# Performance work log

Measured on AMD Instinct MI355X. Metric: run time of the kernel, lower is better.

The kernel has to match this reference:

```python
import jax, jax.numpy as jnp
import numpy as np

NUM_WIRES = 20
BATCH = 32
DIM = 2 ** NUM_WIRES


def setup_inputs() -> dict:
    key = jax.random.key(0)
    k1, k2, k3 = jax.random.split(key, 3)
    state = jax.random.normal(k1, (BATCH, DIM), dtype=jnp.float32)
    state = state / jnp.linalg.norm(state, axis=1, keepdims=True)  # valid quantum states
    params = jax.random.normal(k2, (2 * NUM_WIRES,), dtype=jnp.float32)
    W = jax.random.normal(k3, (1, NUM_WIRES), dtype=jnp.float32) * 0.1
    b = jnp.zeros((1,), dtype=jnp.float32)
    return {"state": state, "params": params, "W": W, "b": b}


def _apply_1q(psi, U, wire):
    # psi: [B, 2^n] complex; apply 2x2 unitary U on `wire` (wire 0 = most significant axis,
    # matching PennyLane's big-endian wire ordering).
    B = psi.shape[0]
    left = 2 ** wire
    psi4 = psi.reshape(B, left, 2, -1)
    psi4 = jnp.einsum('ts,bisj->bitj', U, psi4)
    return psi4.reshape(B, DIM)


def _apply_cnot(psi, ctrl):
    # CNOT on adjacent wires (ctrl, ctrl+1): swap target amplitudes where control=1.
    B = psi.shape[0]
    left = 2 ** ctrl
    psi5 = psi.reshape(B, left, 2, 2, -1)
    top = psi5[:, :, 0]
    bot = psi5[:, :, 1, ::-1]
    return jnp.stack([top, bot], axis=2).reshape(B, DIM)


def _circuit(state, params):
    psi = state.astype(jnp.complex64)
    for i in range(NUM_WIRES):
        # RX(theta_i)
        c = jnp.cos(params[i] / 2).astype(jnp.complex64)
        s = jnp.sin(params[i] / 2)
        RX = jnp.stack([jnp.stack([c, -1j * s]), jnp.stack([-1j * s, c])])
        psi = _apply_1q(psi, RX, i)
        # RY(theta_{i+n})
        c2 = jnp.cos(params[i + NUM_WIRES] / 2).astype(jnp.complex64)
        s2 = jnp.sin(params[i + NUM_WIRES] / 2).astype(jnp.complex64)
        RY = jnp.stack([jnp.stack([c2, -s2]), jnp.stack([s2, c2])])
        psi = _apply_1q(psi, RY, i)
    for i in range(NUM_WIRES - 1):
        psi = _apply_cnot(psi, i)
    # <Z_i> = sum over basis states of |amp|^2 * (+1 if bit_i==0 else -1)
    probs = psi.real ** 2 + psi.imag ** 2  # [B, 2^n] float32
    B = probs.shape[0]
    feats = []
    for i in range(NUM_WIRES):
        p = probs.reshape(B, 2 ** i, 2, -1)
        feats.append(p[:, :, 0].sum(axis=(1, 2)) - p[:, :, 1].sum(axis=(1, 2)))
    return jnp.stack(feats, axis=1)  # [B, n]


def reference(state, params, W, b):
    feats = _circuit(state, params)          # [B, num_wires]
    out = feats @ W.T + b                    # Linear head
    return out.squeeze(-1)                   # [B]
```

## Files before the change

kernel.cpp:

```cpp
#include <hip/hip_runtime.h>
#include <hip/hip_fp16.h>

#define NW    20
#define BATCH 32

struct PkW7 { __half2 a, d, dn, e, en, f, fn, pad; };

__device__ __forceinline__ __half2 pkrtz(float lo, float hi) {
    typedef __fp16 f16x2 __attribute__((ext_vector_type(2)));
    f16x2 v = __builtin_amdgcn_cvt_pkrtz(lo, hi);
    return *reinterpret_cast<__half2*>(&v);
}
__device__ __forceinline__ unsigned h2u(__half2 v) { return *reinterpret_cast<unsigned*>(&v); }
__device__ __forceinline__ __half2 u2h(unsigned v) { return *reinterpret_cast<__half2*>(&v); }

template<int JB>
__device__ __forceinline__ void stage16s(__half2 (&xr)[16], __half2 (&xi)[16], const PkW7 u) {
    #pragma unroll
    for (int base = 0; base < 16; ++base)
        if (!(base & (1 << JB))) {
            const int p = base | (1 << JB);
            __half2 x0r = xr[base], x0i = xi[base], x1r = xr[p], x1i = xi[p];
            xr[base] = __hfma2(u.a, x0r, __hfma2(u.dn, x0i, __hfma2(u.en, x1r, __hmul2(u.f , x1i))));
            xi[base] = __hfma2(u.a, x0i, __hfma2(u.d , x0r, __hfma2(u.en, x1i, __hmul2(u.fn, x1r))));
            xr[p]    = __hfma2(u.e, x0r, __hfma2(u.f , x0i, __hfma2(u.a , x1r, __hmul2(u.d , x1i))));
            xi[p]    = __hfma2(u.e, x0i, __hfma2(u.fn, x0r, __hfma2(u.a , x1i, __hmul2(u.dn, x1r))));
        }
}

__global__ void setupk(const float* __restrict__ params, float* __restrict__ cbuf) {
    int w = threadIdx.x;
    if (w < NW) {
        double s1, c1, s2, c2;
        sincos(0.5 * (double)params[w],      &s1, &c1);
        sincos(0.5 * (double)params[w + NW], &s2, &c2);
        float a = (float)(c1 * c2), d = (float)(s1 * s2);
        float e = (float)(s2 * c1), f = (float)(c2 * s1);
        if (w == 19) {
            cbuf[0] = a * 1024.f; cbuf[1] = d * 1024.f;
            cbuf[2] = e * 1024.f; cbuf[3] = f * 1024.f;
        }
        PkW7 pw;
        pw.a  = __floats2half2_rn( a,  a);
        pw.d  = __floats2half2_rn( d,  d);
        pw.dn = __floats2half2_rn(-d, -d);
        pw.e  = __floats2half2_rn( e,  e);
        pw.en = __floats2half2_rn(-e, -e);
        pw.f  = __floats2half2_rn( f,  f);
        pw.fn = __floats2half2_rn(-f, -f);
        pw.pad = __floats2half2_rn(0.f, 0.f);
        ((PkW7*)(cbuf + 4))[w] = pw;
    }
}

__global__ __launch_bounds__(256, 4) void pass1(const float* __restrict__ state,
                                                const float* __restrict__ cbuf,
                                                uint2* __restrict__ amp) {
    __shared__ __half2 Lr[4224];
    __shared__ __half2 Li[4224];
    const int t     = threadIdx.x;
    const int pr    = blockIdx.x >> 8;
    const int chunk = blockIdx.x & 255;
    const PkW7* PW = (const PkW7*)(cbuf + 4);
    const float a19 = cbuf[0], d19 = cbuf[1], e19 = cbuf[2], f19 = cbuf[3];

    const float4* s0 = (const float4*)(state + ((size_t)pr << 20) + ((size_t)chunk << 12));
    const float4* s1 = (const float4*)((const float*)s0 + ((size_t)16 << 20));

    __half2 xr[16], xi[16];
    #pragma unroll
    for (int k = 0; k < 4; ++k) {
        float4 v0 = s0[k * 256 + t];
        float4 v1 = s1[k * 256 + t];
        float r0a = fmaf(a19, v0.x, -e19 * v0.y), i0a = fmaf( d19, v0.x, -f19 * v0.y);
        float r1a = fmaf(e19, v0.x,  a19 * v0.y), i1a = fmaf(-f19, v0.x, -d19 * v0.y);
        float r0b = fmaf(a19, v1.x, -e19 * v1.y), i0b = fmaf( d19, v1.x, -f19 * v1.y);
        float r1b = fmaf(e19, v1.x,  a19 * v1.y), i1b = fmaf(-f19, v1.x, -d19 * v1.y);
        xr[4*k+0] = pkrtz(r0a, r0b); xi[4*k+0] = pkrtz(i0a, i0b);
        xr[4*k+1] = pkrtz(r1a, r1b); xi[4*k+1] = pkrtz(i1a, i1b);
        r0a = fmaf(a19, v0.z, -e19 * v0.w); i0a = fmaf( d19, v0.z, -f19 * v0.w);
        r1a = fmaf(e19, v0.z,  a19 * v0.w); i1a = fmaf(-f19, v0.z, -d19 * v0.w);
        r0b = fmaf(a19, v1.z, -e19 * v1.w); i0b = fmaf( d19, v1.z, -f19 * v1.w);
        r1b = fmaf(e19, v1.z,  a19 * v1.w); i1b = fmaf(-f19, v1.z, -d19 * v1.w);
        xr[4*k+2] = pkrtz(r0a, r0b); xi[4*k+2] = pkrtz(i0a, i0b);
        xr[4*k+3] = pkrtz(r1a, r1b); xi[4*k+3] = pkrtz(i1a, i1b);
    }
    stage16s<1>(xr, xi, PW[18]);
    stage16s<2>(xr, xi, PW[9]);
    stage16s<3>(xr, xi, PW[8]);
    {
        const int p1 = 4 * t + (t >> 3);
        #pragma unroll
        for (int r = 0; r < 16; ++r) {
            const int a = p1 + (r & 3) + 1056 * (r >> 2);
            Lr[a] = xr[r]; Li[a] = xi[r];
        }
    }
    __syncthreads();

    const int p2 = (t & 3) + 66 * (t >> 2);
    #pragma unroll
    for (int r = 0; r < 16; ++r) {
        const int c = 4 * (r & 3) + 16 * (r >> 2);
        const int a = p2 + c + (c >> 5);
        xr[r] = Lr[a]; xi[r] = Li[a];
    }
    stage16s<0>(xr, xi, PW[17]);
    stage16s<1>(xr, xi, PW[16]);
    stage16s<2>(xr, xi, PW[15]);
    stage16s<3>(xr, xi, PW[14]);
    #pragma unroll
    for (int r = 0; r < 16; ++r) {
        const int c = 4 * (r & 3) + 16 * (r >> 2);
        const int a = p2 + c + (c >> 5);
        Lr[a] = xr[r]; Li[a] = xi[r];
    }
    __syncthreads();

    const int p3 = (t & 63) + ((t & 63) >> 5) + 1056 * (t >> 6);
    #pragma unroll
    for (int r = 0; r < 16; ++r) {
        const int a = p3 + 66 * (r & 3) + 264 * (r >> 2);
        xr[r] = Lr[a]; xi[r] = Li[a];
    }
    stage16s<0>(xr, xi, PW[13]);
    stage16s<1>(xr, xi, PW[12]);
    stage16s<2>(xr, xi, PW[11]);
    stage16s<3>(xr, xi, PW[10]);

    uint2* dst = amp + ((size_t)pr << 20) + ((size_t)chunk << 12);
    const int sbase = (t & 63) + 1024 * (t >> 6);
    #pragma unroll
    for (int r = 0; r < 16; ++r) {
        uint2 w; w.x = h2u(xr[r]); w.y = h2u(xi[r]);
        dst[sbase + 64 * (r & 3) + 256 * (r >> 2)] = w;
    }
}

__global__ __launch_bounds__(256, 4) void pass2(const uint2* __restrict__ amp,
                                                const float* __restrict__ cbuf,
                                                const float* __restrict__ Wv,
                                                float* __restrict__ pws) {
    __shared__ __half2 Lr[4224];
    __shared__ __half2 Li[4224];
    __shared__ float2  Asig[256];
    __shared__ float   Btab[16];
    __shared__ float   wred[8];
    const int t        = threadIdx.x;
    const int pr       = blockIdx.x >> 8;
    const int chunk    = blockIdx.x & 255;
    const int low_base = chunk * 16;
    const int l = t & 15, hi = t >> 4;
    const PkW7* PW = (const PkW7*)(cbuf + 4);

    {
        float A = 0.f;
        #pragma unroll
        for (int i = 0; i < 8; ++i)
            A += Wv[i] * (1.f - 2.f * (float)(__popc(t >> (7 - i)) & 1));
        Asig[t] = make_float2(A, 1.f - 2.f * (float)(__popc(t) & 1));
    }
    if (t < 16) {
        int low = low_base + t;
        float Bs = 0.f;
        #pragma unroll
        for (int i = 8; i < 20; ++i)
            Bs += Wv[i] * (1.f - 2.f * (float)(__popc(low >> (19 - i)) & 1));
        Btab[t] = Bs;
    }

    const uint2* src = amp + ((size_t)pr << 20) + low_base + l;
    __half2 xr[16], xi[16];
    #pragma unroll
    for (int r = 0; r < 16; ++r) {
        uint2 w = src[(size_t)(hi * 16 + r) * 4096];
        xr[r] = u2h(w.x); xi[r] = u2h(w.y);
    }
    stage16s<0>(xr, xi, PW[7]);
    stage16s<1>(xr, xi, PW[6]);
    stage16s<2>(xr, xi, PW[5]);
    stage16s<3>(xr, xi, PW[4]);
    {
        const int p = 264 * hi + l;
        #pragma unroll
        for (int r = 0; r < 16; ++r) {
            const int a = p + 16 * r + (r >> 1);
            Lr[a] = xr[r]; Li[a] = xi[r];
        }
    }
    __syncthreads();
    {
        const int p = t + (t >> 5);
        #pragma unroll
        for (int r = 0; r < 16; ++r) {
            const int a = p + 264 * r;
            xr[r] = Lr[a]; xi[r] = Li[a];
        }
    }
    stage16s<0>(xr, xi, PW[3]);
    stage16s<1>(xr, xi, PW[2]);
    stage16s<2>(xr, xi, PW[1]);
    stage16s<3>(xr, xi, PW[0]);

    const float Bl = Btab[l];
    float acc0 = 0.f, acc1 = 0.f;
    #pragma unroll
    for (int r = 0; r < 16; ++r) {
        float2 vr = __half22float2(xr[r]);
        float2 vi = __half22float2(xi[r]);
        float2 as = Asig[r * 16 + hi];
        float g = fmaf(as.y, Bl, as.x);
        acc0 = fmaf(fmaf(vr.x, vr.x, vi.x * vi.x), g, acc0);
        acc1 = fmaf(fmaf(vr.y, vr.y, vi.y * vi.y), g, acc1);
    }
    #pragma unroll
    for (int off = 32; off > 0; off >>= 1) {
        acc0 += __shfl_down(acc0, off, 64);
        acc1 += __shfl_down(acc1, off, 64);
    }
    if ((t & 63) == 0) { wred[(t >> 6) * 2] = acc0; wred[(t >> 6) * 2 + 1] = acc1; }
    __syncthreads();
    if (t < 2)
        pws[blockIdx.x * 2 + t] = (wred[t] + wred[2 + t]) + (wred[4 + t] + wred[6 + t]);
}

__global__ void finalk(const float* __restrict__ pws, const float* __restrict__ bias,
                       float* __restrict__ out) {
    const int t = threadIdx.x;
    const int b = t >> 3, j = t & 7;
    const int pr = b & 15, sl = b >> 4;
    float s = 0.f;
    #pragma unroll 4
    for (int k = 0; k < 32; ++k) {
        const int c = j * 32 + k;
        s += pws[(pr * 256 + c) * 2 + sl];
    }
    s += __shfl_down(s, 4, 8);
    s += __shfl_down(s, 2, 8);
    s += __shfl_down(s, 1, 8);
    if (j == 0) out[b] = s * (1.f / 1048576.f) + bias[0];
}

extern "C" void kernel_launch(void* const* d_in, const int* in_sizes, int n_in,
                              void* d_out, int out_size, void* d_ws, size_t ws_size,
                              hipStream_t stream) {
    const float* state  = (const float*)d_in[0];
    const float* params = (const float*)d_in[1];
    const float* Wv     = (const float*)d_in[2];
    const float* bias   = (const float*)d_in[3];
    float* out = (float*)d_out;

    uint2* amp  = (uint2*)d_ws;
    float* pws  = (float*)((char*)d_ws + (size_t)16 * (1u << 20) * 8);
    float* cbuf = (float*)((char*)d_ws + (size_t)16 * (1u << 20) * 8 + 8192 * 4);

    setupk<<<1, 64, 0, stream>>>(params, cbuf);
    pass1 <<<16 * 256, 256, 0, stream>>>(state, cbuf, amp);
    pass2 <<<16 * 256, 256, 0, stream>>>(amp, cbuf, Wv, pws);
    finalk<<<1, 256, 0, stream>>>(pws, bias, out);
}
```

Measured before the change: 107.2 us.

## Halve per-thread register tile to 8 amplitudes and rebalance wire split across passes

Each thread now holds 8 packed complex amplitudes instead of 16, and shared memory per block is halved. Block count doubles and launch bounds ask for 8 blocks per SM. The wire partition moves to 11 wires in pass1 and 9 in pass2, so both passes get new shared-memory transpose layouts, a three-stage exchange, and new reduction tables. The aim is higher occupancy and fewer registers to hide memory latency, at the cost of an extra barrier round and more, smaller blocks.

After: 155.0 us. +44.6%, slower.

```diff
diff --git a/kernel.cpp b/kernel.cpp
--- a/kernel.cpp
+++ b/kernel.cpp
@@ -1,8 +1,7 @@
 #include <hip/hip_runtime.h>
 #include <hip/hip_fp16.h>
 
-#define NW    20
-#define BATCH 32
+#define NW 20
 
 struct PkW7 { __half2 a, d, dn, e, en, f, fn, pad; };
 
@@ -15,9 +14,9 @@
 __device__ __forceinline__ __half2 u2h(unsigned v) { return *reinterpret_cast<__half2*>(&v); }
 
 template<int JB>
-__device__ __forceinline__ void stage16s(__half2 (&xr)[16], __half2 (&xi)[16], const PkW7 u) {
-    #pragma unroll
-    for (int base = 0; base < 16; ++base)
+__device__ __forceinline__ void stage8s(__half2 (&xr)[8], __half2 (&xi)[8], const PkW7 u) {
+    #pragma unroll
+    for (int base = 0; base < 8; ++base)
         if (!(base & (1 << JB))) {
             const int p = base | (1 << JB);
             __half2 x0r = xr[base], x0i = xi[base], x1r = xr[p], x1i = xi[p];
@@ -53,23 +52,23 @@
     }
 }
 
-__global__ __launch_bounds__(256, 4) void pass1(const float* __restrict__ state,
+__global__ __launch_bounds__(256, 8) void pass1(const float* __restrict__ state,
                                                 const float* __restrict__ cbuf,
                                                 uint2* __restrict__ amp) {
-    __shared__ __half2 Lr[4224];
-    __shared__ __half2 Li[4224];
+    __shared__ __half2 Lr[2112];
+    __shared__ __half2 Li[2112];
     const int t     = threadIdx.x;
-    const int pr    = blockIdx.x >> 8;
-    const int chunk = blockIdx.x & 255;
+    const int pr    = blockIdx.x >> 9;
+    const int chunk = blockIdx.x & 511;
     const PkW7* PW = (const PkW7*)(cbuf + 4);
     const float a19 = cbuf[0], d19 = cbuf[1], e19 = cbuf[2], f19 = cbuf[3];
 
-    const float4* s0 = (const float4*)(state + ((size_t)pr << 20) + ((size_t)chunk << 12));
+    const float4* s0 = (const float4*)(state + ((size_t)pr << 20) + ((size_t)chunk << 11));
     const float4* s1 = (const float4*)((const float*)s0 + ((size_t)16 << 20));
 
-    __half2 xr[16], xi[16];
-    #pragma unroll
-    for (int k = 0; k < 4; ++k) {
+    __half2 xr[8], xi[8];
+    #pragma unroll
+    for (int k = 0; k < 2; ++k) {
         float4 v0 = s0[k * 256 + t];
         float4 v1 = s1[k * 256 + t];
         float r0a = fmaf(a19, v0.x, -e19 * v0.y), i0a = fmaf( d19, v0.x, -f19 * v0.y);
@@ -85,131 +84,126 @@
         xr[4*k+2] = pkrtz(r0a, r0b); xi[4*k+2] = pkrtz(i0a, i0b);
         xr[4*k+3] = pkrtz(r1a, r1b); xi[4*k+3] = pkrtz(i1a, i1b);
     }
-    stage16s<1>(xr, xi, PW[18]);
-    stage16s<2>(xr, xi, PW[9]);
-    stage16s<3>(xr, xi, PW[8]);
+    stage8s<1>(xr, xi, PW[18]);
+    stage8s<2>(xr, xi, PW[9]);
     {
         const int p1 = 4 * t + (t >> 3);
         #pragma unroll
-        for (int r = 0; r < 16; ++r) {
+        for (int r = 0; r < 8; ++r) {
             const int a = p1 + (r & 3) + 1056 * (r >> 2);
             Lr[a] = xr[r]; Li[a] = xi[r];
         }
     }
     __syncthreads();
 
-    const int p2 = (t & 3) + 66 * (t >> 2);
-    #pragma unroll
-    for (int r = 0; r < 16; ++r) {
-        const int c = 4 * (r & 3) + 16 * (r >> 2);
-        const int a = p2 + c + (c >> 5);
-        xr[r] = Lr[a]; xi[r] = Li[a];
-    }
-    stage16s<0>(xr, xi, PW[17]);
-    stage16s<1>(xr, xi, PW[16]);
-    stage16s<2>(xr, xi, PW[15]);
-    stage16s<3>(xr, xi, PW[14]);
-    #pragma unroll
-    for (int r = 0; r < 16; ++r) {
-        const int c = 4 * (r & 3) + 16 * (r >> 2);
-        const int a = p2 + c + (c >> 5);
-        Lr[a] = xr[r]; Li[a] = xi[r];
-    }
-    __syncthreads();
-
-    const int p3 = (t & 63) + ((t & 63) >> 5) + 1056 * (t >> 6);
-    #pragma unroll
-    for (int r = 0; r < 16; ++r) {
-        const int a = p3 + 66 * (r & 3) + 264 * (r >> 2);
-        xr[r] = Lr[a]; xi[r] = Li[a];
-    }
-    stage16s<0>(xr, xi, PW[13]);
-    stage16s<1>(xr, xi, PW[12]);
-    stage16s<2>(xr, xi, PW[11]);
-    stage16s<3>(xr, xi, PW[10]);
-
-    uint2* dst = amp + ((size_t)pr << 20) + ((size_t)chunk << 12);
-    const int sbase = (t & 63) + 1024 * (t >> 6);
-    #pragma unroll
-    for (int r = 0; r < 16; ++r) {
+    const int q2 = (t & 3) + 33 * (t >> 2);
+    #pragma unroll
+    for (int r = 0; r < 8; ++r) { xr[r] = Lr[q2 + 4*r]; xi[r] = Li[q2 + 4*r]; }
+    stage8s<0>(xr, xi, PW[17]);
+    stage8s<1>(xr, xi, PW[16]);
+    stage8s<2>(xr, xi, PW[15]);
+    #pragma unroll
+    for (int r = 0; r < 8; ++r) { Lr[q2 + 4*r] = xr[r]; Li[q2 + 4*r] = xi[r]; }
+    __syncthreads();
+
+    const int q3 = (t & 31) + 264 * (t >> 5);
+    #pragma unroll
+    for (int r = 0; r < 8; ++r) { xr[r] = Lr[q3 + 33*r]; xi[r] = Li[q3 + 33*r]; }
+    stage8s<0>(xr, xi, PW[14]);
+    stage8s<1>(xr, xi, PW[13]);
+    stage8s<2>(xr, xi, PW[12]);
+    #pragma unroll
+    for (int r = 0; r < 8; ++r) { Lr[q3 + 33*r] = xr[r]; Li[q3 + 33*r] = xi[r]; }
+    __syncthreads();
+
+    const int q4 = t + (t >> 5);
+    #pragma unroll
+    for (int r = 0; r < 8; ++r) { xr[r] = Lr[q4 + 264*r]; xi[r] = Li[q4 + 264*r]; }
+    stage8s<0>(xr, xi, PW[11]);
+    stage8s<1>(xr, xi, PW[10]);
+
+    uint2* dst = amp + ((((size_t)pr << 9) | (size_t)chunk) << 11);
+    #pragma unroll
+    for (int r = 0; r < 8; ++r) {
         uint2 w; w.x = h2u(xr[r]); w.y = h2u(xi[r]);
-        dst[sbase + 64 * (r & 3) + 256 * (r >> 2)] = w;
-    }
-}
-
-__global__ __launch_bounds__(256, 4) void pass2(const uint2* __restrict__ amp,
+        dst[t + 256 * r] = w;
+    }
+}
+
+__global__ __launch_bounds__(256, 8) void pass2(const uint2* __restrict__ amp,
                                                 const float* __restrict__ cbuf,
                                                 const float* __restrict__ Wv,
                                                 float* __restrict__ pws) {
-    __shared__ __half2 Lr[4224];
-    __shared__ __half2 Li[4224];
-    __shared__ float2  Asig[256];
-    __shared__ float   Btab[16];
+    __shared__ __half2 Lr[2112];
+    __shared__ __half2 Li[2112];
+    __shared__ float   Atab[512];
+    __shared__ float   Btab[4];
     __shared__ float   wred[8];
-    const int t        = threadIdx.x;
-    const int pr       = blockIdx.x >> 8;
-    const int chunk    = blockIdx.x & 255;
-    const int low_base = chunk * 16;
-    const int l = t & 15, hi = t >> 4;
+    const int t  = threadIdx.x;
+    const int pr = blockIdx.x >> 9;
+    const int cb = blockIdx.x & 511;
     const PkW7* PW = (const PkW7*)(cbuf + 4);
 
-    {
+    #pragma unroll
+    for (int hh = t; hh < 512; hh += 256) {
         float A = 0.f;
         #pragma unroll
-        for (int i = 0; i < 8; ++i)
-            A += Wv[i] * (1.f - 2.f * (float)(__popc(t >> (7 - i)) & 1));
-        Asig[t] = make_float2(A, 1.f - 2.f * (float)(__popc(t) & 1));
-    }
-    if (t < 16) {
-        int low = low_base + t;
+        for (int i = 0; i < 9; ++i)
+            A += Wv[i] * (1.f - 2.f * (float)(__popc(hh >> (8 - i)) & 1));
+        Atab[hh] = A;
+    }
+    if (t < 4) {
+        int low = cb * 4 + t;
         float Bs = 0.f;
         #pragma unroll
-        for (int i = 8; i < 20; ++i)
+        for (int i = 9; i < 20; ++i)
             Bs += Wv[i] * (1.f - 2.f * (float)(__popc(low >> (19 - i)) & 1));
         Btab[t] = Bs;
     }
 
-    const uint2* src = amp + ((size_t)pr << 20) + low_base + l;
-    __half2 xr[16], xi[16];
-    #pragma unroll
-    for (int r = 0; r < 16; ++r) {
-        uint2 w = src[(size_t)(hi * 16 + r) * 4096];
+    const uint2* src = amp + ((size_t)pr << 20) + ((size_t)(t >> 2) << 14) + (cb << 2) + (t & 3);
+    __half2 xr[8], xi[8];
+    #pragma unroll
+    for (int r = 0; r < 8; ++r) {
+        uint2 w = src[r << 11];
         xr[r] = u2h(w.x); xi[r] = u2h(w.y);
     }
-    stage16s<0>(xr, xi, PW[7]);
-    stage16s<1>(xr, xi, PW[6]);
-    stage16s<2>(xr, xi, PW[5]);
-    stage16s<3>(xr, xi, PW[4]);
+    stage8s<0>(xr, xi, PW[8]);
+    stage8s<1>(xr, xi, PW[7]);
+    stage8s<2>(xr, xi, PW[6]);
     {
-        const int p = 264 * hi + l;
-        #pragma unroll
-        for (int r = 0; r < 16; ++r) {
-            const int a = p + 16 * r + (r >> 1);
-            Lr[a] = xr[r]; Li[a] = xi[r];
-        }
-    }
-    __syncthreads();
-    {
-        const int p = t + (t >> 5);
-        #pragma unroll
-        for (int r = 0; r < 16; ++r) {
-            const int a = p + 264 * r;
-            xr[r] = Lr[a]; xi[r] = Li[a];
-        }
-    }
-    stage16s<0>(xr, xi, PW[3]);
-    stage16s<1>(xr, xi, PW[2]);
-    stage16s<2>(xr, xi, PW[1]);
-    stage16s<3>(xr, xi, PW[0]);
-
-    const float Bl = Btab[l];
+        const int w1 = (t & 3) + 33 * (t >> 2);
+        #pragma unroll
+        for (int r = 0; r < 8; ++r) { Lr[w1 + 4*r] = xr[r]; Li[w1 + 4*r] = xi[r]; }
+    }
+    __syncthreads();
+
+    const int q2 = (t & 31) + 264 * (t >> 5);
+    #pragma unroll
+    for (int r = 0; r < 8; ++r) { xr[r] = Lr[q2 + 33*r]; xi[r] = Li[q2 + 33*r]; }
+    stage8s<0>(xr, xi, PW[5]);
+    stage8s<1>(xr, xi, PW[4]);
+    stage8s<2>(xr, xi, PW[3]);
+    #pragma unroll
+    for (int r = 0; r < 8; ++r) { Lr[q2 + 33*r] = xr[r]; Li[q2 + 33*r] = xi[r]; }
+    __syncthreads();
+
+    const int q3 = t + (t >> 5);
+    #pragma unroll
+    for (int r = 0; r < 8; ++r) { xr[r] = Lr[q3 + 264*r]; xi[r] = Li[q3 + 264*r]; }
+    stage8s<0>(xr, xi, PW[2]);
+    stage8s<1>(xr, xi, PW[1]);
+    stage8s<2>(xr, xi, PW[0]);
+
+    const float Bl = Btab[t & 3];
     float acc0 = 0.f, acc1 = 0.f;
     #pragma unroll
-    for (int r = 0; r < 16; ++r) {
+    for (int r = 0; r < 8; ++r) {
+        const int h = (t >> 2) + 64 * r;
+        const float sg = 1.f - 2.f * (float)(__popc(h) & 1);
+        const float g  = fmaf(sg, Bl, Atab[h]);
         float2 vr = __half22float2(xr[r]);
         float2 vi = __half22float2(xi[r]);
-        float2 as = Asig[r * 16 + hi];
-        float g = fmaf(as.y, Bl, as.x);
         acc0 = fmaf(fmaf(vr.x, vr.x, vi.x * vi.x), g, acc0);
         acc1 = fmaf(fmaf(vr.y, vr.y, vi.y * vi.y), g, acc1);
     }
@@ -231,9 +225,9 @@
     const int pr = b & 15, sl = b >> 4;
     float s = 0.f;
     #pragma unroll 4
-    for (int k = 0; k < 32; ++k) {
-        const int c = j * 32 + k;
-        s += pws[(pr * 256 + c) * 2 + sl];
+    for (int k = 0; k < 64; ++k) {
+        const int cb = j * 64 + k;
+        s += pws[(pr * 512 + cb) * 2 + sl];
     }
     s += __shfl_down(s, 4, 8);
     s += __shfl_down(s, 2, 8);
@@ -250,12 +244,13 @@
     const float* bias   = (const float*)d_in[3];
     float* out = (float*)d_out;
 
+    const size_t AMPB = (size_t)16 * (1u << 20) * 8;
     uint2* amp  = (uint2*)d_ws;
-    float* pws  = (float*)((char*)d_ws + (size_t)16 * (1u << 20) * 8);
-    float* cbuf = (float*)((char*)d_ws + (size_t)16 * (1u << 20) * 8 + 8192 * 4);
+    float* pws  = (float*)((char*)d_ws + AMPB);
+    float* cbuf = (float*)((char*)d_ws + AMPB + 65536);
 
     setupk<<<1, 64, 0, stream>>>(params, cbuf);
-    pass1 <<<16 * 256, 256, 0, stream>>>(state, cbuf, amp);
-    pass2 <<<16 * 256, 256, 0, stream>>>(amp, cbuf, Wv, pws);
+    pass1 <<<16 * 512, 256, 0, stream>>>(state, cbuf, amp);
+    pass2 <<<16 * 512, 256, 0, stream>>>(amp, cbuf, Wv, pws);
     finalk<<<1, 256, 0, stream>>>(pws, bias, out);
 }
```
